# Performance work log

Measured on AMD Instinct MI355X. Metric: run time of the kernel, lower is better.

Reference implementation:

```python
import jax, jax.numpy as jnp
import numpy as np
import math

B, S, IN, H, M = 4, 2048, 256, 128, 128  # mem_dim must equal hidden_size


def _xavier(key, shape):
    fan_in, fan_out = shape[0], shape[-1]
    lim = math.sqrt(6.0 / (fan_in + fan_out))
    return jax.random.uniform(key, shape, jnp.float32, -lim, lim)


def setup_inputs() -> dict:
    key = jax.random.key(0)
    ks = jax.random.split(key, 8)
    return dict(
        x=jax.random.normal(ks[0], (B, S, IN), jnp.float32),
        c0=jnp.zeros((M, M), jnp.float32),   # init_hidden matrix memory
        n0=jnp.zeros((M, 1), jnp.float32),   # init_hidden normalizer
        w_q=_xavier(ks[1], (IN, H)), b_q=jnp.zeros((H,), jnp.float32),
        w_k=_xavier(ks[2], (IN, M)), b_k=jnp.zeros((M,), jnp.float32),
        w_v=_xavier(ks[3], (IN, M)), b_v=jnp.zeros((M,), jnp.float32),
        w_i=_xavier(ks[4], (IN, 1)), b_i=jnp.zeros((1,), jnp.float32),
        w_f=_xavier(ks[5], (IN, 1)), b_f=jnp.zeros((1,), jnp.float32),
        w_o=_xavier(ks[6], (IN, H)), b_o=jnp.zeros((H,), jnp.float32),
    )


def reference(x, c0, n0, w_q, b_q, w_k, b_k, w_v, b_v, w_i, b_i, w_f, b_f, w_o, b_o):
    Bb, Ss, Ii = x.shape
    Mm = w_k.shape[1]
    Hh = w_q.shape[1]
    xf = x.reshape(Bb * Ss, Ii)                                  # [N, IN]
    q = xf @ w_q + b_q                                           # [N, H]
    k = (xf @ w_k + b_k) * (1.0 / math.sqrt(Mm))                 # [N, M]
    v = xf @ w_v + b_v                                           # [N, M]
    i_t = jnp.exp(xf @ w_i + b_i)                                # [N, 1]
    f_t = jax.nn.sigmoid(xf @ w_f + b_f)                         # [N, 1]
    # Original loop never updates c_prev: c_t[n] = f[n]*c0 + i[n]*outer(v[n], k[n])
    c = f_t[:, :, None] * c0[None] + i_t[:, :, None] * (v[:, :, None] * k[:, None, :])  # [N, M, M]
    n = f_t[:, :, None] * n0[None] + i_t[:, :, None] * k[:, :, None]                    # [N, M, 1]
    c = c.reshape(Bb, Ss, Mm, Mm)
    n = n.reshape(Bb, Ss, Mm, 1)
    q4 = q.reshape(Bb, Ss, Hh)
    nq = jnp.einsum('bsm,bsm->bs', n[..., 0], q4)                # n^T q
    denom = jnp.maximum(jnp.abs(nq), 1.0)[..., None]             # max(|n^T q|, 1)
    h_tilde = jnp.einsum('bsmk,bsk->bsm', c, q4) / denom         # (c_t q) / denom
    o = jax.nn.sigmoid(xf @ w_o + b_o).reshape(Bb, Ss, Hh)
    h = o * h_tilde                                              # [B, S, H]
    return (h, c, n)
```

## Files before the change

kernel.cpp:

```cpp
#include <hip/hip_runtime.h>
#include <math.h>

#define B_    4
#define S_    2048
#define IN_   256
#define H_    128
#define M_    128
#define NROWS (B_ * S_)
#define RPB   16
#define TPB   256
#define XPAD  260

typedef float f4_t __attribute__((ext_vector_type(4)));

__global__ __launch_bounds__(TPB, 3) void xlstm_proj(
    const float* __restrict__ x,
    const float* __restrict__ c0,
    const float* __restrict__ n0,
    const float* __restrict__ w_q, const float* __restrict__ b_q,
    const float* __restrict__ w_k, const float* __restrict__ b_k,
    const float* __restrict__ w_v, const float* __restrict__ b_v,
    const float* __restrict__ w_i, const float* __restrict__ b_i,
    const float* __restrict__ w_f, const float* __restrict__ b_f,
    const float* __restrict__ w_o, const float* __restrict__ b_o,
    float* __restrict__ out_h,
    float* __restrict__ out_n,
    float* __restrict__ kws,
    float* __restrict__ vws,
    float* __restrict__ ifws)
{
    __shared__ float xs[RPB][XPAD];
    __shared__ float qs[RPB][M_];
    __shared__ float ks[RPB][M_];
    __shared__ float vs[RPB][M_];
    __shared__ float os_[RPB][M_];
    __shared__ float itf[RPB][2];
    __shared__ float scal[RPB][2];

    const int t    = threadIdx.x;
    const int row0 = blockIdx.x * RPB;

    for (int p4 = t; p4 < RPB * IN_ / 4; p4 += TPB) {
        int p = p4 * 4;
        float4 v = *(const float4*)(x + (size_t)row0 * IN_ + p);
        int r = p >> 8, c = p & 255;
        *(float4*)&xs[r][c] = v;
    }
    __syncthreads();

    const int col   = t & 127;
    const int kh    = t >> 7;
    const int kbase = kh << 7;

    float accq[16], acck[16], accv[16], acco[16];
    #pragma unroll
    for (int r = 0; r < 16; ++r) { accq[r]=0.f; acck[r]=0.f; accv[r]=0.f; acco[r]=0.f; }

    #pragma unroll 2
    for (int k4 = 0; k4 < 128; k4 += 4) {
        const int wi = (kbase + k4) * H_ + col;
        float4 wq, wk, wv, wo;
        wq.x = w_q[wi]; wq.y = w_q[wi + H_]; wq.z = w_q[wi + 2*H_]; wq.w = w_q[wi + 3*H_];
        wk.x = w_k[wi]; wk.y = w_k[wi + M_]; wk.z = w_k[wi + 2*M_]; wk.w = w_k[wi + 3*M_];
        wv.x = w_v[wi]; wv.y = w_v[wi + M_]; wv.z = w_v[wi + 2*M_]; wv.w = w_v[wi + 3*M_];
        wo.x = w_o[wi]; wo.y = w_o[wi + H_]; wo.z = w_o[wi + 2*H_]; wo.w = w_o[wi + 3*H_];

        #pragma unroll
        for (int r = 0; r < 16; ++r) {
            float4 xr = *(const float4*)&xs[r][kbase + k4];
            accq[r] = fmaf(xr.x, wq.x, fmaf(xr.y, wq.y, fmaf(xr.z, wq.z, fmaf(xr.w, wq.w, accq[r]))));
            acck[r] = fmaf(xr.x, wk.x, fmaf(xr.y, wk.y, fmaf(xr.z, wk.z, fmaf(xr.w, wk.w, acck[r]))));
            accv[r] = fmaf(xr.x, wv.x, fmaf(xr.y, wv.y, fmaf(xr.z, wv.z, fmaf(xr.w, wv.w, accv[r]))));
            acco[r] = fmaf(xr.x, wo.x, fmaf(xr.y, wo.y, fmaf(xr.z, wo.z, fmaf(xr.w, wo.w, acco[r]))));
        }
    }

    if (kh == 1) {
        #pragma unroll
        for (int r = 0; r < 16; ++r) {
            qs[r][col]  = accq[r];
            ks[r][col]  = acck[r];
            vs[r][col]  = accv[r];
            os_[r][col] = acco[r];
        }
    }
    __syncthreads();
    if (kh == 0) {
        const float kscale = 0.08838834764831843f;
        #pragma unroll
        for (int r = 0; r < 16; ++r) {
            float q  = accq[r] + qs[r][col] + b_q[col];
            float kk = (acck[r] + ks[r][col] + b_k[col]) * kscale;
            float vv = accv[r] + vs[r][col] + b_v[col];
            float oo = acco[r] + os_[r][col] + b_o[col];
            qs[r][col]  = q;
            ks[r][col]  = kk;
            vs[r][col]  = vv;
            os_[r][col] = 1.f / (1.f + __expf(-oo));
        }
    }
    __syncthreads();

    {
        const int gr = t >> 4, gseg = t & 15;
        const float* xrow = &xs[gr][gseg * 16];
        float pi = 0.f, pf = 0.f;
        #pragma unroll
        for (int u = 0; u < 4; ++u) {
            float4 xv  = *(const float4*)(xrow + u * 4);
            float4 wiv = *(const float4*)(w_i + gseg * 16 + u * 4);
            float4 wfv = *(const float4*)(w_f + gseg * 16 + u * 4);
            pi = fmaf(xv.x, wiv.x, fmaf(xv.y, wiv.y, fmaf(xv.z, wiv.z, fmaf(xv.w, wiv.w, pi))));
            pf = fmaf(xv.x, wfv.x, fmaf(xv.y, wfv.y, fmaf(xv.z, wfv.z, fmaf(xv.w, wfv.w, pf))));
        }
        #pragma unroll
        for (int m = 1; m < 16; m <<= 1) { pi += __shfl_xor(pi, m); pf += __shfl_xor(pf, m); }
        if (gseg == 0) {
            itf[gr][0] = __expf(pi + b_i[0]);
            itf[gr][1] = 1.f / (1.f + __expf(-(pf + b_f[0])));
        }
    }

    const int rbase = kh * 8;
    float c0qr[8];
    {
        #pragma unroll
        for (int r = 0; r < 8; ++r) c0qr[r] = 0.f;
        const float* c0row = c0 + (size_t)col * M_;
        #pragma unroll 2
        for (int j4 = 0; j4 < M_; j4 += 4) {
            float4 w4 = *(const float4*)(c0row + j4);
            #pragma unroll
            for (int r = 0; r < 8; ++r) {
                float4 q4 = *(const float4*)&qs[rbase + r][j4];
                c0qr[r] = fmaf(w4.x, q4.x, fmaf(w4.y, q4.y, fmaf(w4.z, q4.z, fmaf(w4.w, q4.w, c0qr[r]))));
            }
        }
    }

    {
        const int gr = t >> 4, gseg = t & 15;
        const int j0 = gseg * 8;
        float pkq = 0.f, pnq = 0.f;
        #pragma unroll
        for (int u = 0; u < 2; ++u) {
            float4 kk = *(const float4*)&ks[gr][j0 + u * 4];
            float4 qq = *(const float4*)&qs[gr][j0 + u * 4];
            float4 nn = *(const float4*)(n0 + j0 + u * 4);
            pkq = fmaf(kk.x, qq.x, fmaf(kk.y, qq.y, fmaf(kk.z, qq.z, fmaf(kk.w, qq.w, pkq))));
            pnq = fmaf(nn.x, qq.x, fmaf(nn.y, qq.y, fmaf(nn.z, qq.z, fmaf(nn.w, qq.w, pnq))));
        }
        #pragma unroll
        for (int m = 1; m < 16; m <<= 1) { pkq += __shfl_xor(pkq, m); pnq += __shfl_xor(pnq, m); }
        if (gseg == 0) { scal[gr][0] = pkq; scal[gr][1] = pnq; }
    }
    __syncthreads();

    #pragma unroll
    for (int r = 0; r < 8; ++r) {
        int row = rbase + r;
        size_t grow = (size_t)(row0 + row);
        float iv = itf[row][0], fv = itf[row][1];
        float kv = ks[row][col];
        out_n[grow * M_ + col] = fmaf(fv, n0[col], iv * kv);
        float nq    = fmaf(fv, scal[row][1], iv * scal[row][0]);
        float denom = fmaxf(fabsf(nq), 1.0f);
        float ht = fmaf(fv, c0qr[r], iv * vs[row][col] * scal[row][0]) / denom;
        out_h[grow * H_ + col] = os_[row][col] * ht;
        kws[grow * M_ + col] = kv;
        vws[grow * M_ + col] = vs[row][col];
    }
    if (t < 32) {
        int r = t & 15;
        size_t grow = (size_t)(row0 + r);
        if (t < 16) ifws[grow * 2 + 0] = itf[r][0];
        else        ifws[grow * 2 + 1] = itf[r][1];
    }
}

__global__ __launch_bounds__(TPB) void xlstm_cstream(
    const float* __restrict__ c0,
    const float* __restrict__ kws,
    const float* __restrict__ vws,
    const float* __restrict__ ifws,
    float* __restrict__ out_c)
{
    const int t    = threadIdx.x;
    const int row0 = blockIdx.x * RPB;

    __shared__ float vsh[RPB][M_];
    __shared__ float ksh[RPB][M_];
    __shared__ float2 ish[RPB];

    for (int p4 = t; p4 < RPB * M_ / 4; p4 += TPB) {
        int idx = p4 * 4;
        int r = idx >> 7, c = idx & 127;
        *(float4*)&vsh[r][c] = *(const float4*)(vws + (size_t)row0 * M_ + idx);
        *(float4*)&ksh[r][c] = *(const float4*)(kws + (size_t)row0 * M_ + idx);
    }
    if (t < RPB) ish[t] = *(const float2*)(ifws + (size_t)(row0 + t) * 2);
    __syncthreads();

    const int base = t * 4;
    const int j    = base & 127;

    float ivr[RPB], fvr[RPB];
    float4 kreg[RPB];
    #pragma unroll
    for (int r = 0; r < RPB; ++r) {
        ivr[r] = ish[r].x; fvr[r] = ish[r].y;
        kreg[r] = *(const float4*)&ksh[r][j];
    }

    #pragma unroll 2
    for (int ch = 0; ch < 16; ++ch) {
        int p = (ch << 10) + base;
        int m = p >> 7;
        float4 c0v = *(const float4*)(c0 + p);
        #pragma unroll
        for (int r = 0; r < RPB; ++r) {
            float s = ivr[r] * vsh[r][m];
            f4_t o4;
            o4.x = fmaf(fvr[r], c0v.x, s * kreg[r].x);
            o4.y = fmaf(fvr[r], c0v.y, s * kreg[r].y);
            o4.z = fmaf(fvr[r], c0v.z, s * kreg[r].z);
            o4.w = fmaf(fvr[r], c0v.w, s * kreg[r].w);
            __builtin_nontemporal_store(o4,
                (f4_t*)(out_c + (size_t)(row0 + r) * (M_ * M_) + p));
        }
    }
}

extern "C" void kernel_launch(void* const* d_in, const int* in_sizes, int n_in,
                              void* d_out, int out_size, void* d_ws, size_t ws_size,
                              hipStream_t stream) {
    const float* x   = (const float*)d_in[0];
    const float* c0  = (const float*)d_in[1];
    const float* n0  = (const float*)d_in[2];
    const float* w_q = (const float*)d_in[3];  const float* b_q = (const float*)d_in[4];
    const float* w_k = (const float*)d_in[5];  const float* b_k = (const float*)d_in[6];
    const float* w_v = (const float*)d_in[7];  const float* b_v = (const float*)d_in[8];
    const float* w_i = (const float*)d_in[9];  const float* b_i = (const float*)d_in[10];
    const float* w_f = (const float*)d_in[11]; const float* b_f = (const float*)d_in[12];
    const float* w_o = (const float*)d_in[13]; const float* b_o = (const float*)d_in[14];

    float* out   = (float*)d_out;
    float* out_h = out;
    float* out_c = out + (size_t)NROWS * H_;
    float* out_n = out_c + (size_t)NROWS * M_ * M_;

    float* kws  = (float*)d_ws;
    float* vws  = kws + (size_t)NROWS * M_;
    float* ifws = vws + (size_t)NROWS * M_;

    hipLaunchKernelGGL(xlstm_proj, dim3(NROWS / RPB), dim3(TPB), 0, stream,
                       x, c0, n0, w_q, b_q, w_k, b_k, w_v, b_v,
                       w_i, b_i, w_f, b_f, w_o, b_o,
                       out_h, out_n, kws, vws, ifws);

    hipLaunchKernelGGL(xlstm_cstream, dim3(NROWS / RPB), dim3(TPB), 0, stream,
                       c0, kws, vws, ifws, out_c);
}
```

Before: 156.5 us.

## Restructure c-stream kernel to hold c0 in registers and loop over rows

The output-c streaming kernel now processes 8 rows per block instead of 16, doubling the grid. Each thread loads its slice of c0 into registers once and then iterates over rows, writing each row's contiguous 64KB slab in turn, where before it iterated over c0 chunks with all rows inside. The nontemporal stores are replaced with ordinary stores. This is meant to cut register pressure from the per-row k/i/f arrays and to make the write stream more sequential. The cost is that c0 gets reloaded by twice as many blocks, and output writes may now pollute the cache.

```diff
diff --git a/kernel.cpp b/kernel.cpp
--- a/kernel.cpp
+++ b/kernel.cpp
@@ -8,6 +8,7 @@
 #define M_    128
 #define NROWS (B_ * S_)
 #define RPB   16
+#define SRPB  8
 #define TPB   256
 #define XPAD  260
 
@@ -186,47 +187,43 @@
     float* __restrict__ out_c)
 {
     const int t    = threadIdx.x;
-    const int row0 = blockIdx.x * RPB;
-
-    __shared__ float vsh[RPB][M_];
-    __shared__ float ksh[RPB][M_];
-    __shared__ float2 ish[RPB];
-
-    for (int p4 = t; p4 < RPB * M_ / 4; p4 += TPB) {
-        int idx = p4 * 4;
+    const int row0 = blockIdx.x * SRPB;
+
+    __shared__ float vsh[SRPB][M_];
+    __shared__ float ksh[SRPB][M_];
+    __shared__ float2 ish[SRPB];
+
+    {
+        int idx = t * 4;
         int r = idx >> 7, c = idx & 127;
         *(float4*)&vsh[r][c] = *(const float4*)(vws + (size_t)row0 * M_ + idx);
         *(float4*)&ksh[r][c] = *(const float4*)(kws + (size_t)row0 * M_ + idx);
     }
-    if (t < RPB) ish[t] = *(const float2*)(ifws + (size_t)(row0 + t) * 2);
-    __syncthreads();
-
-    const int base = t * 4;
-    const int j    = base & 127;
-
-    float ivr[RPB], fvr[RPB];
-    float4 kreg[RPB];
+    if (t < SRPB) ish[t] = *(const float2*)(ifws + (size_t)(row0 + t) * 2);
+
+    float4 c0r[16];
     #pragma unroll
-    for (int r = 0; r < RPB; ++r) {
-        ivr[r] = ish[r].x; fvr[r] = ish[r].y;
-        kreg[r] = *(const float4*)&ksh[r][j];
-    }
-
-    #pragma unroll 2
-    for (int ch = 0; ch < 16; ++ch) {
-        int p = (ch << 10) + base;
-        int m = p >> 7;
-        float4 c0v = *(const float4*)(c0 + p);
-        #pragma unroll
-        for (int r = 0; r < RPB; ++r) {
-            float s = ivr[r] * vsh[r][m];
-            f4_t o4;
-            o4.x = fmaf(fvr[r], c0v.x, s * kreg[r].x);
-            o4.y = fmaf(fvr[r], c0v.y, s * kreg[r].y);
-            o4.z = fmaf(fvr[r], c0v.z, s * kreg[r].z);
-            o4.w = fmaf(fvr[r], c0v.w, s * kreg[r].w);
-            __builtin_nontemporal_store(o4,
-                (f4_t*)(out_c + (size_t)(row0 + r) * (M_ * M_) + p));
+    for (int ch = 0; ch < 16; ++ch)
+        c0r[ch] = *(const float4*)(c0 + (ch << 10) + t * 4);
+    __syncthreads();
+
+    const int j    = (t * 4) & 127;
+    const int msub = t >> 5;
+
+    #pragma unroll 1
+    for (int r = 0; r < SRPB; ++r) {
+        const float4 k4 = *(const float4*)&ksh[r][j];
+        const float  iv = ish[r].x, fv = ish[r].y;
+        float* outr = out_c + (size_t)(row0 + r) * (M_ * M_);
+        #pragma unroll
+        for (int ch = 0; ch < 16; ++ch) {
+            float s = iv * vsh[r][(ch << 3) + msub];
+            float4 o4;
+            o4.x = fmaf(fv, c0r[ch].x, s * k4.x);
+            o4.y = fmaf(fv, c0r[ch].y, s * k4.y);
+            o4.z = fmaf(fv, c0r[ch].z, s * k4.z);
+            o4.w = fmaf(fv, c0r[ch].w, s * k4.w);
+            *(float4*)(outr + (ch << 10) + t * 4) = o4;
         }
     }
 }
@@ -258,6 +255,6 @@
                        w_i, b_i, w_f, b_f, w_o, b_o,
                        out_h, out_n, kws, vws, ifws);
 
-    hipLaunchKernelGGL(xlstm_cstream, dim3(NROWS / RPB), dim3(TPB), 0, stream,
+    hipLaunchKernelGGL(xlstm_cstream, dim3(NROWS / SRPB), dim3(TPB), 0, stream,
                        c0, kws, vws, ifws, out_c);
 }
```

Measured after the change: 229.6 us. 46.7% more time.
